# Kernel optimization log

Measured on AMD Instinct MI355X. Metric: run time of the kernel, lower is better.

The kernel has to match this reference:

```python
import jax, jax.numpy as jnp
import numpy as np

N, E, G = 50000, 800000, 512
F_IN, ED, NUM_CLASSES = 128, 3, 10
H1, C1, C2 = 4, 32, 64


def _add_self_loops(src, dst, eattr, n):
    # PyG add_self_loops with fill_value='mean': loop attr = mean of incoming edge attrs
    cnt = jax.ops.segment_sum(jnp.ones_like(dst, dtype=eattr.dtype), dst, num_segments=n)
    loop = jax.ops.segment_sum(eattr, dst, num_segments=n) / jnp.maximum(cnt, 1.0)[:, None]
    ar = jnp.arange(n)
    return (jnp.concatenate([src, ar]), jnp.concatenate([dst, ar]),
            jnp.concatenate([eattr, loop], axis=0))


def _gatv2(x, src, dst, eattr, Wl, bl, Wr, br, We, att, bias, heads, out_ch, concat, n):
    xl = (x @ Wl.T + bl).reshape(n, heads, out_ch)   # source transform (lin_l)
    xr = (x @ Wr.T + br).reshape(n, heads, out_ch)   # target transform (lin_r)
    ee = (eattr @ We.T).reshape(-1, heads, out_ch)   # edge transform (lin_edge, no bias)
    m = jax.nn.leaky_relu(xl[src] + xr[dst] + ee, 0.2)  # [E', H, C]
    score = jnp.einsum('ehc,hc->eh', m, att)
    # segment softmax over incoming edges of each target node
    smax = jax.ops.segment_max(score, dst, num_segments=n)
    ex = jnp.exp(score - smax[dst])
    denom = jax.ops.segment_sum(ex, dst, num_segments=n)
    alpha = ex / denom[dst]
    out = jax.ops.segment_sum(alpha[:, :, None] * xl[src], dst, num_segments=n)
    out = out.reshape(n, heads * out_ch) if concat else out.mean(axis=1)
    return out + bias


def setup_inputs() -> dict:
    key = jax.random.key(0)
    ks = jax.random.split(key, 24)
    s = 0.1
    return {
        'x': jax.random.normal(ks[0], (N, F_IN), jnp.float32),
        'edge_index': jax.random.randint(ks[1], (2, E), 0, N),
        'edge_attr': jax.random.normal(ks[2], (E, ED), jnp.float32),
        'batch': jnp.sort(jax.random.randint(ks[3], (N,), 0, G)),
        'u': jax.random.normal(ks[4], (G, 1), jnp.float32),
        'Wl1': jax.random.normal(ks[5], (H1 * C1, F_IN), jnp.float32) * s,
        'bl1': jnp.zeros((H1 * C1,), jnp.float32),
        'Wr1': jax.random.normal(ks[6], (H1 * C1, F_IN), jnp.float32) * s,
        'br1': jnp.zeros((H1 * C1,), jnp.float32),
        'We1': jax.random.normal(ks[7], (H1 * C1, ED), jnp.float32) * s,
        'att1': jax.random.normal(ks[8], (H1, C1), jnp.float32) * s,
        'b1': jnp.zeros((H1 * C1,), jnp.float32),
        'Wl2': jax.random.normal(ks[9], (C2, H1 * C1), jnp.float32) * s,
        'bl2': jnp.zeros((C2,), jnp.float32),
        'Wr2': jax.random.normal(ks[10], (C2, H1 * C1), jnp.float32) * s,
        'br2': jnp.zeros((C2,), jnp.float32),
        'We2': jax.random.normal(ks[11], (C2, ED), jnp.float32) * s,
        'att2': jax.random.normal(ks[12], (1, C2), jnp.float32) * s,
        'b2': jnp.zeros((C2,), jnp.float32),
        'W_lin1': jax.random.normal(ks[13], (32, 65), jnp.float32) * s,
        'b_lin1': jnp.zeros((32,), jnp.float32),
        'W_head': jax.random.normal(ks[14], (NUM_CLASSES, 32), jnp.float32) * s,
        'b_head': jnp.zeros((NUM_CLASSES,), jnp.float32),
    }


def reference(x, edge_index, edge_attr, batch, u,
              Wl1, bl1, Wr1, br1, We1, att1, b1,
              Wl2, bl2, Wr2, br2, We2, att2, b2,
              W_lin1, b_lin1, W_head, b_head):
    n = x.shape[0]
    src, dst, ea = _add_self_loops(edge_index[0], edge_index[1], edge_attr, n)
    h = jax.nn.elu(_gatv2(x, src, dst, ea, Wl1, bl1, Wr1, br1, We1, att1, b1, H1, C1, True, n))
    h = jax.nn.elu(_gatv2(h, src, dst, ea, Wl2, bl2, Wr2, br2, We2, att2, b2, 1, C2, False, n))
    cnt = jax.ops.segment_sum(jnp.ones((n,), h.dtype), batch, num_segments=G)
    pooled = jax.ops.segment_sum(h, batch, num_segments=G) / jnp.maximum(cnt, 1.0)[:, None]
    z = jax.nn.relu(jnp.concatenate([pooled, u], axis=1) @ W_lin1.T + b_lin1)
    return z @ W_head.T + b_head
```

## Files before the change

### kernel.cpp

```cpp
#include <hip/hip_runtime.h>
#include <hip/hip_fp16.h>
#include <math.h>


union H2U { __half2 h; unsigned u; };
typedef _Float16 hv2_t __attribute__((ext_vector_type(2)));
typedef unsigned uv4_t __attribute__((ext_vector_type(4)));

__device__ __forceinline__ __half2 hmax2(__half2 a, __half2 b) {
  union { __half2 h; hv2_t v; } x, y, r;
  x.h = a; y.h = b;
  r.v = __builtin_elementwise_max(x.v, y.v);
  return r.h;
}

#if __has_builtin(__builtin_amdgcn_fdot2)
__device__ __forceinline__ float dot2f(__half2 a, __half2 b, float c) {
  union { __half2 h; hv2_t v; } x, y;
  x.h = a; y.h = b;
  return __builtin_amdgcn_fdot2(x.v, y.v, c, false);
}
#else
__device__ __forceinline__ float dot2f(__half2 a, __half2 b, float c) {
  float2 af = __half22float2(a), bf = __half22float2(b);
  return fmaf(af.x, bf.x, fmaf(af.y, bf.y, c));
}
#endif

#if __has_builtin(__builtin_amdgcn_exp2f)
__device__ __forceinline__ float fexp2(float x) { return __builtin_amdgcn_exp2f(x); }
#else
__device__ __forceinline__ float fexp2(float x) { return exp2f(x); }
#endif

#if __has_builtin(__builtin_amdgcn_update_dpp)
template <int CTRL>
__device__ __forceinline__ float dpp_add(float v) {
  int r = __builtin_amdgcn_update_dpp(0, __builtin_bit_cast(int, v),
                                      CTRL, 0xf, 0xf, true);
  return v + __builtin_bit_cast(float, r);
}
__device__ __forceinline__ float row_sum16(float v) {
  v = dpp_add<0x121>(v);
  v = dpp_add<0x122>(v);
  v = dpp_add<0x124>(v);
  v = dpp_add<0x128>(v);
  return v;
}
#else
__device__ __forceinline__ float row_sum16(float v) {
  v += __shfl_xor(v, 1);
  v += __shfl_xor(v, 2);
  v += __shfl_xor(v, 4);
  v += __shfl_xor(v, 8);
  return v;
}
#endif

__device__ __forceinline__ float lowf(unsigned u) {
  H2U t; t.u = u;
  return __half2float(__low2half(t.h));
}

#define LOG2E 1.44269504088896f

__global__ void hist_k(const int* __restrict__ dst, int* __restrict__ deg,
                       int* __restrict__ rank, int E) {
  int e = blockIdx.x * 256 + threadIdx.x;
  if (e < E) rank[e] = atomicAdd(&deg[dst[e]], 1);
}

__global__ void blocksum_k(const int* __restrict__ deg, int* __restrict__ bsum, int N) {
  __shared__ int s[256];
  int i = blockIdx.x * 256 + threadIdx.x;
  s[threadIdx.x] = (i < N) ? deg[i] : 0;
  __syncthreads();
  for (int off = 128; off; off >>= 1) {
    if (threadIdx.x < off) s[threadIdx.x] += s[threadIdx.x + off];
    __syncthreads();
  }
  if (threadIdx.x == 0) bsum[blockIdx.x] = s[0];
}

__global__ void writeptr_k(const int* __restrict__ deg, const int* __restrict__ bsum,
                           int* __restrict__ rowptr, int N, int E) {
  __shared__ int s[256];
  __shared__ int bs[256];
  int t = threadIdx.x;
  int i = blockIdx.x * 256 + t;
  bs[t] = (t < (int)blockIdx.x) ? bsum[t] : 0;
  s[t] = (i < N) ? deg[i] : 0;
  __syncthreads();
  for (int off = 128; off; off >>= 1) {
    if (t < off) bs[t] += bs[t + off];
    __syncthreads();
  }
  int base = bs[0];
  __syncthreads();
  for (int off = 1; off < 256; off <<= 1) {
    int v = (t >= off) ? s[t - off] : 0;
    __syncthreads();
    if (t >= off) s[t] += v;
    __syncthreads();
  }
  int excl = base + ((t == 0) ? 0 : s[t - 1]) + i;
  if (i < N) rowptr[i] = excl;
  if (i == N - 1) rowptr[N] = E + N;
}

__global__ void fill_k(const int* __restrict__ src, const int* __restrict__ dst,
                       const float* __restrict__ eattr, const int* __restrict__ rowptr,
                       const int* __restrict__ rank, uint4* __restrict__ erec, int E) {
  int e = blockIdx.x * 256 + threadIdx.x;
  if (e >= E) return;
  int pos = rowptr[dst[e]] + rank[e];
  H2U a0, a1, a2;
  float e0 = eattr[e * 3 + 0], e1 = eattr[e * 3 + 1], e2 = eattr[e * 3 + 2];
  a0.h = __floats2half2_rn(e0, e0);
  a1.h = __floats2half2_rn(e1, e1);
  a2.h = __floats2half2_rn(e2, e2);
  uv4_t v = {(unsigned)src[e], a0.u, a1.u, a2.u};
  __builtin_nontemporal_store(v, (uv4_t*)&erec[pos]);
}

__global__ void loopattr_k(const int* __restrict__ rowptr, uint4* __restrict__ erec, int N) {
  int lane = threadIdx.x & 63;
  int n = (int)((blockIdx.x * 256 + threadIdx.x) >> 6);
  if (n >= N) return;
  int beg = rowptr[n], endr = rowptr[n + 1] - 1;
  float f0 = 0.f, f1 = 0.f, f2 = 0.f;
  for (int i = beg + lane; i < endr; i += 64) {
    uint4 r = erec[i];
    f0 += lowf(r.y);
    f1 += lowf(r.z);
    f2 += lowf(r.w);
  }
#pragma unroll
  for (int off = 1; off < 64; off <<= 1) {
    f0 += __shfl_xor(f0, off);
    f1 += __shfl_xor(f1, off);
    f2 += __shfl_xor(f2, off);
  }
  if (lane == 0) {
    float inv = 1.0f / fmaxf((float)(endr - beg), 1.0f);
    H2U a0, a1, a2;
    a0.h = __floats2half2_rn(f0 * inv, f0 * inv);
    a1.h = __floats2half2_rn(f1 * inv, f1 * inv);
    a2.h = __floats2half2_rn(f2 * inv, f2 * inv);
    erec[endr] = make_uint4((unsigned)n, a0.u, a1.u, a2.u);
  }
}

template <int J>
__global__ __launch_bounds__(256) void node_linear2t_k(
    const float* __restrict__ X,
    const float* __restrict__ W1, const float* __restrict__ b1v,
    const float* __restrict__ W2, const float* __restrict__ b2v,
    __half* __restrict__ out1, __half* __restrict__ out2, int nrows) {
  constexpr int K = 128, KB = 32;
  constexpr int JG = J / 4;
  constexpr int RG = 256 / JG;
  constexpr int RB = RG * 8;
  constexpr int XP2 = RB + 4;
  constexpr int WP2 = J + 4;
  __shared__ __align__(16) __half2 sXT2[K / 2][XP2];
  __shared__ __align__(16) __half2 sW1T2[KB / 2][WP2];
  __shared__ __align__(16) __half2 sW2T2[KB / 2][WP2];

  int tid = threadIdx.x;
  int n0 = blockIdx.x * RB;

  {
    int r = tid & (RB - 1);
    constexpr int KQSX = 256 / RB;
    int n = n0 + r;
    bool ok = n < nrows;
    for (int kq = tid / RB; kq < K / 4; kq += KQSX) {
      float4 v = ok ? *(const float4*)&X[(size_t)n * K + kq * 4]
                    : make_float4(0.f, 0.f, 0.f, 0.f);
      sXT2[kq * 2 + 0][r] = __floats2half2_rn(v.x, v.y);
      sXT2[kq * 2 + 1][r] = __floats2half2_rn(v.z, v.w);
    }
  }

  int jg = tid % JG;
  int rg = tid / JG;
  float acc1[8][4] = {}, acc2[8][4] = {};

  for (int kb = 0; kb < K / KB; ++kb) {
    __syncthreads();
    {
      int j = tid & (J - 1);
      constexpr int KQS = 256 / J;
      for (int kq = tid / J; kq < KB / 4; kq += KQS) {
        float4 v1 = *(const float4*)&W1[(size_t)j * K + kb * KB + kq * 4];
        float4 v2 = *(const float4*)&W2[(size_t)j * K + kb * KB + kq * 4];
        sW1T2[kq * 2 + 0][j] = __floats2half2_rn(v1.x, v1.y);
        sW1T2[kq * 2 + 1][j] = __floats2half2_rn(v1.z, v1.w);
        sW2T2[kq * 2 + 0][j] = __floats2half2_rn(v2.x, v2.y);
        sW2T2[kq * 2 + 1][j] = __floats2half2_rn(v2.z, v2.w);
      }
    }
    __syncthreads();
#pragma unroll
    for (int k2 = 0; k2 < KB / 2; ++k2) {
      __half2 xs2[8], w1s2[4], w2s2[4];
      *(float4*)&xs2[0] = *(const float4*)&sXT2[kb * (KB / 2) + k2][rg * 8];
      *(float4*)&xs2[4] = *(const float4*)&sXT2[kb * (KB / 2) + k2][rg * 8 + 4];
      *(float4*)w1s2 = *(const float4*)&sW1T2[k2][jg * 4];
      *(float4*)w2s2 = *(const float4*)&sW2T2[k2][jg * 4];
#pragma unroll
      for (int i = 0; i < 8; ++i)
#pragma unroll
        for (int q = 0; q < 4; ++q) {
          acc1[i][q] = dot2f(xs2[i], w1s2[q], acc1[i][q]);
          acc2[i][q] = dot2f(xs2[i], w2s2[q], acc2[i][q]);
        }
    }
  }

  float4 bv1 = *(const float4*)&b1v[jg * 4];
  float4 bv2 = *(const float4*)&b2v[jg * 4];
#pragma unroll
  for (int i = 0; i < 8; ++i) {
    int n = n0 + rg * 8 + i;
    if (n < nrows) {
      H2U a, b, c, d;
      a.h = __floats2half2_rn(acc1[i][0] + bv1.x, acc1[i][1] + bv1.y);
      b.h = __floats2half2_rn(acc1[i][2] + bv1.z, acc1[i][3] + bv1.w);
      *(uint2*)&out1[(size_t)n * J + jg * 4] = make_uint2(a.u, b.u);
      c.h = __floats2half2_rn(acc2[i][0] + bv2.x, acc2[i][1] + bv2.y);
      d.h = __floats2half2_rn(acc2[i][2] + bv2.z, acc2[i][3] + bv2.w);
      *(uint2*)&out2[(size_t)n * J + jg * 4] = make_uint2(c.u, d.u);
    }
  }
}

__global__ __launch_bounds__(128) void gat1_fused_k(
    const int* __restrict__ rowptr, const uint4* __restrict__ erec,
    const __half* __restrict__ xlh, const __half* __restrict__ xrh,
    const float* __restrict__ We, const float* __restrict__ att,
    const float* __restrict__ bias, float* __restrict__ out, int N) {
  constexpr int CH = 8;
  int lane = threadIdx.x & 63;
  int wave0 = __builtin_amdgcn_readfirstlane(
      (int)((blockIdx.x * blockDim.x + threadIdx.x) >> 6));
  int nwaves = (gridDim.x * blockDim.x) >> 6;
  const __half2* xl2p = (const __half2*)xlh;
  const __half2* xr2p = (const __half2*)xrh;
  int c0 = 2 * lane;
  __half2 w0p = __floats2half2_rn(We[c0 * 3 + 0], We[c0 * 3 + 3]);
  __half2 w1p = __floats2half2_rn(We[c0 * 3 + 1], We[c0 * 3 + 4]);
  __half2 w2p = __floats2half2_rn(We[c0 * 3 + 2], We[c0 * 3 + 5]);
  __half2 attp = __floats2half2_rn(att[c0] * LOG2E, att[c0 + 1] * LOG2E);
  __half2 k02 = __floats2half2_rn(0.2f, 0.2f);
  float2 bv = make_float2(bias[c0], bias[c0 + 1]);

  for (int n = wave0; n < N; n += nwaves) {
    __half2 xrp = xr2p[(size_t)n * 64 + lane];
    int beg = rowptr[n], end = rowptr[n + 1];
    int cnt = end - beg;

    float acc0 = 0.f, acc1 = 0.f, den = 0.f;

    int nfull = cnt / CH;
    for (int ch = 0; ch < nfull; ++ch) {
      int b = beg + ch * CH;
      uint4 recs[CH];
#pragma unroll
      for (int j = 0; j < CH; ++j) recs[j] = erec[b + j];
      __half2 r_[CH];
#pragma unroll
      for (int j = 0; j < CH; ++j) {
        int s = __builtin_amdgcn_readfirstlane((int)recs[j].x);
        r_[j] = xl2p[(size_t)s * 64 + lane];
      }
#pragma unroll
      for (int j = 0; j < CH; ++j) {
        H2U e0, e1, e2;
        e0.u = recs[j].y; e1.u = recs[j].z; e2.u = recs[j].w;
        __half2 m = __hadd2(r_[j], xrp);
        m = __hfma2(e0.h, w0p, m);
        m = __hfma2(e1.h, w1p, m);
        m = __hfma2(e2.h, w2p, m);
        m = hmax2(m, __hmul2(m, k02));
        float v = row_sum16(dot2f(m, attp, 0.f));
        float ex = fexp2(v);
        float2 rfF = __half22float2(r_[j]);
        den += ex;
        acc0 = fmaf(ex, rfF.x, acc0);
        acc1 = fmaf(ex, rfF.y, acc1);
      }
    }
    int gi = beg + nfull * CH;
    for (; gi + 2 <= end; gi += 2) {
      uint4 recA = erec[gi];
      uint4 recB = erec[gi + 1];
      int sA = __builtin_amdgcn_readfirstlane((int)recA.x);
      int sB = __builtin_amdgcn_readfirstlane((int)recB.x);
      __half2 rfA = xl2p[(size_t)sA * 64 + lane];
      __half2 rfB = xl2p[(size_t)sB * 64 + lane];
      {
        H2U e0, e1, e2;
        e0.u = recA.y; e1.u = recA.z; e2.u = recA.w;
        __half2 m = __hadd2(rfA, xrp);
        m = __hfma2(e0.h, w0p, m);
        m = __hfma2(e1.h, w1p, m);
        m = __hfma2(e2.h, w2p, m);
        m = hmax2(m, __hmul2(m, k02));
        float v = row_sum16(dot2f(m, attp, 0.f));
        float ex = fexp2(v);
        float2 rfF = __half22float2(rfA);
        den += ex;
        acc0 = fmaf(ex, rfF.x, acc0);
        acc1 = fmaf(ex, rfF.y, acc1);
      }
      {
        H2U e0, e1, e2;
        e0.u = recB.y; e1.u = recB.z; e2.u = recB.w;
        __half2 m = __hadd2(rfB, xrp);
        m = __hfma2(e0.h, w0p, m);
        m = __hfma2(e1.h, w1p, m);
        m = __hfma2(e2.h, w2p, m);
        m = hmax2(m, __hmul2(m, k02));
        float v = row_sum16(dot2f(m, attp, 0.f));
        float ex = fexp2(v);
        float2 rfF = __half22float2(rfB);
        den += ex;
        acc0 = fmaf(ex, rfF.x, acc0);
        acc1 = fmaf(ex, rfF.y, acc1);
      }
    }
    if (gi < end) {
      uint4 rec = erec[gi];
      int s = __builtin_amdgcn_readfirstlane((int)rec.x);
      __half2 rf = xl2p[(size_t)s * 64 + lane];
      H2U e0, e1, e2;
      e0.u = rec.y; e1.u = rec.z; e2.u = rec.w;
      __half2 m = __hadd2(rf, xrp);
      m = __hfma2(e0.h, w0p, m);
      m = __hfma2(e1.h, w1p, m);
      m = __hfma2(e2.h, w2p, m);
      m = hmax2(m, __hmul2(m, k02));
      float v = row_sum16(dot2f(m, attp, 0.f));
      float ex = fexp2(v);
      float2 rfF = __half22float2(rf);
      den += ex;
      acc0 = fmaf(ex, rfF.x, acc0);
      acc1 = fmaf(ex, rfF.y, acc1);
    }

    float o0 = acc0 / den + bv.x;
    float o1 = acc1 / den + bv.y;
    o0 = o0 > 0.f ? o0 : __expf(o0) - 1.0f;
    o1 = o1 > 0.f ? o1 : __expf(o1) - 1.0f;
    *(float2*)&out[(size_t)n * 128 + c0] = make_float2(o0, o1);
  }
}

__global__ __launch_bounds__(128) void gat2_fused_k(
    const int* __restrict__ rowptr, const uint4* __restrict__ erec,
    const __half* __restrict__ xlh, const __half* __restrict__ xrh,
    const float* __restrict__ We, const float* __restrict__ att,
    const float* __restrict__ bias, float* __restrict__ out, int N) {
  constexpr int CP = 4;
  int lane = threadIdx.x & 63;
  int wave0 = __builtin_amdgcn_readfirstlane(
      (int)((blockIdx.x * blockDim.x + threadIdx.x) >> 6));
  int nwaves = (gridDim.x * blockDim.x) >> 6;
  int sub = lane & 31, grp = lane >> 5;
  int c0 = 2 * sub;
  const __half2* xl2p = (const __half2*)xlh;
  const __half2* xr2p = (const __half2*)xrh;
  __half2 w0p = __floats2half2_rn(We[c0 * 3 + 0], We[c0 * 3 + 3]);
  __half2 w1p = __floats2half2_rn(We[c0 * 3 + 1], We[c0 * 3 + 4]);
  __half2 w2p = __floats2half2_rn(We[c0 * 3 + 2], We[c0 * 3 + 5]);
  __half2 attp = __floats2half2_rn(att[c0] * LOG2E, att[c0 + 1] * LOG2E);
  __half2 k02 = __floats2half2_rn(0.2f, 0.2f);
  float2 bv = make_float2(bias[c0], bias[c0 + 1]);

  for (int n = wave0; n < N; n += nwaves) {
    __half2 xrp = xr2p[(size_t)n * 32 + sub];
    int beg = rowptr[n], end = rowptr[n + 1];
    int cnt = end - beg;

    float acc0 = 0.f, acc1 = 0.f, den = 0.f;

    int nfull = cnt / (2 * CP);
    int b = beg + grp;
    for (int ch = 0; ch < nfull; ++ch) {
      uint4 recs[CP];
      __half2 r_[CP];
#pragma unroll
      for (int j = 0; j < CP; ++j) recs[j] = erec[b + 2 * j];
#pragma unroll
      for (int j = 0; j < CP; ++j) r_[j] = xl2p[(size_t)recs[j].x * 32 + sub];
#pragma unroll
      for (int j = 0; j < CP; ++j) {
        H2U e0, e1, e2;
        e0.u = recs[j].y; e1.u = recs[j].z; e2.u = recs[j].w;
        __half2 m = __hadd2(r_[j], xrp);
        m = __hfma2(e0.h, w0p, m);
        m = __hfma2(e1.h, w1p, m);
        m = __hfma2(e2.h, w2p, m);
        m = hmax2(m, __hmul2(m, k02));
        float v = row_sum16(dot2f(m, attp, 0.f));
        v += __shfl_xor(v, 16);
        float ex = fexp2(v);
        float2 rfF = __half22float2(r_[j]);
        den += ex;
        acc0 = fmaf(ex, rfF.x, acc0);
        acc1 = fmaf(ex, rfF.y, acc1);
      }
      b += 2 * CP;
    }
    for (int gi = beg + nfull * 2 * CP + grp; gi < end; gi += 2) {
      uint4 rec = erec[gi];
      __half2 rf = xl2p[(size_t)rec.x * 32 + sub];
      H2U e0, e1, e2;
      e0.u = rec.y; e1.u = rec.z; e2.u = rec.w;
      __half2 m = __hadd2(rf, xrp);
      m = __hfma2(e0.h, w0p, m);
      m = __hfma2(e1.h, w1p, m);
      m = __hfma2(e2.h, w2p, m);
      m = hmax2(m, __hmul2(m, k02));
      float v = row_sum16(dot2f(m, attp, 0.f));
      v += __shfl_xor(v, 16);
      float ex = fexp2(v);
      float2 rfF = __half22float2(rf);
      den += ex;
      acc0 = fmaf(ex, rfF.x, acc0);
      acc1 = fmaf(ex, rfF.y, acc1);
    }

    acc0 += __shfl_xor(acc0, 32);
    acc1 += __shfl_xor(acc1, 32);
    den += __shfl_xor(den, 32);

    if (grp == 0) {
      float o0 = acc0 / den + bv.x;
      float o1 = acc1 / den + bv.y;
      o0 = o0 > 0.f ? o0 : __expf(o0) - 1.0f;
      o1 = o1 > 0.f ? o1 : __expf(o1) - 1.0f;
      *(float2*)&out[(size_t)n * 64 + c0] = make_float2(o0, o1);
    }
  }
}

__global__ void final_mlp_k(const float* __restrict__ h2, const int* __restrict__ batch,
                            int N, const float* __restrict__ u,
                            const float* __restrict__ W1, const float* __restrict__ b1,
                            const float* __restrict__ Wh, const float* __restrict__ bh,
                            float* __restrict__ out) {
  __shared__ float comb[4][64];
  __shared__ float feat[65];
  __shared__ float z[32];
  int g = blockIdx.x;
  int t = threadIdx.x;
  int c = t & 63, q = t >> 6;
  int lo, hi;
  {
    int l = 0, h = N;
    while (l < h) { int m = (l + h) >> 1; if (batch[m] < g) l = m + 1; else h = m; }
    lo = l;
    h = N;
    while (l < h) { int m = (l + h) >> 1; if (batch[m] < g + 1) l = m + 1; else h = m; }
    hi = l;
  }
  float a = 0.f;
  for (int nn = lo + q; nn < hi; nn += 4) a += h2[(size_t)nn * 64 + c];
  comb[q][c] = a;
  __syncthreads();
  if (t < 64) {
    float s = comb[0][t] + comb[1][t] + comb[2][t] + comb[3][t];
    float inv = 1.0f / fmaxf((float)(hi - lo), 1.0f);
    feat[t] = s * inv;
    if (t == 0) feat[64] = u[g];
  }
  __syncthreads();
  if (t < 32) {
    float s = b1[t];
    for (int k = 0; k < 65; ++k) s += feat[k] * W1[t * 65 + k];
    z[t] = fmaxf(s, 0.0f);
  }
  __syncthreads();
  if (t < 10) {
    float s = bh[t];
    for (int k = 0; k < 32; ++k) s += z[k] * Wh[t * 32 + k];
    out[g * 10 + t] = s;
  }
}

extern "C" void kernel_launch(void* const* d_in, const int* in_sizes, int n_in,
                              void* d_out, int out_size, void* d_ws, size_t ws_size,
                              hipStream_t stream) {
  const float* x      = (const float*)d_in[0];
  const int*   eidx   = (const int*)d_in[1];
  const float* eattr  = (const float*)d_in[2];
  const int*   batch  = (const int*)d_in[3];
  const float* u      = (const float*)d_in[4];
  const float* Wl1    = (const float*)d_in[5];
  const float* bl1    = (const float*)d_in[6];
  const float* Wr1    = (const float*)d_in[7];
  const float* br1    = (const float*)d_in[8];
  const float* We1    = (const float*)d_in[9];
  const float* att1   = (const float*)d_in[10];
  const float* b1     = (const float*)d_in[11];
  const float* Wl2    = (const float*)d_in[12];
  const float* bl2    = (const float*)d_in[13];
  const float* Wr2    = (const float*)d_in[14];
  const float* br2    = (const float*)d_in[15];
  const float* We2    = (const float*)d_in[16];
  const float* att2   = (const float*)d_in[17];
  const float* b2     = (const float*)d_in[18];
  const float* W_lin1 = (const float*)d_in[19];
  const float* b_lin1 = (const float*)d_in[20];
  const float* W_head = (const float*)d_in[21];
  const float* b_head = (const float*)d_in[22];

  const int N = in_sizes[0] / 128;
  const int E = in_sizes[1] / 2;
  const int G = in_sizes[4];
  const int* srcp = eidx;
  const int* dstp = eidx + E;

  __half* bufh = (__half*)d_ws;
  __half* bufr = bufh + (size_t)N * 128;
  float* buf3 = (float*)(bufr + (size_t)N * 128);
  uint4* erec = (uint4*)(buf3 + (size_t)N * 128);
  int* rank   = (int*)(erec + ((size_t)E + N));
  int* deg    = rank + E;
  int* rowptr = deg + N;
  int* bsum   = rowptr + N + 1;

  const int nb = (N + 255) / 256;
  const int gat_blocks = (N + 1) / 2;

  (void)hipMemsetAsync(deg, 0, sizeof(int) * (size_t)N, stream);
  hist_k<<<(E + 255) / 256, 256, 0, stream>>>(dstp, deg, rank, E);
  blocksum_k<<<nb, 256, 0, stream>>>(deg, bsum, N);
  writeptr_k<<<nb, 256, 0, stream>>>(deg, bsum, rowptr, N, E);
  fill_k<<<(E + 255) / 256, 256, 0, stream>>>(srcp, dstp, eattr, rowptr, rank, erec, E);
  loopattr_k<<<(N * 64 + 255) / 256, 256, 0, stream>>>(rowptr, erec, N);

  node_linear2t_k<128><<<(N + 63) / 64, 256, 0, stream>>>(x, Wl1, bl1, Wr1, br1,
                                                          bufh, bufr, N);
  gat1_fused_k<<<gat_blocks, 128, 0, stream>>>(rowptr, erec, bufh, bufr,
                                               We1, att1, b1, buf3, N);

  node_linear2t_k<64><<<(N + 127) / 128, 256, 0, stream>>>(buf3, Wl2, bl2, Wr2, br2,
                                                           bufh, bufr, N);
  gat2_fused_k<<<gat_blocks, 128, 0, stream>>>(rowptr, erec, bufh, bufr,
                                               We2, att2, b2, buf3, N);

  final_mlp_k<<<G, 256, 0, stream>>>(buf3, batch, N, u, W_lin1, b_lin1, W_head, b_head,
                                     (float*)d_out);
}
```

Before: 366.2 us.

## Replace dot2 node linear kernels with MFMA fp16 matmuls and half-precision intermediates

Replaces the shared-memory dot2-based dual linear kernel with an MFMA 16x16x32 fp16 kernel that reads fp16 inputs and fp16 pre-converted weights straight from global memory. Extra kernels convert x and the four weight matrices to fp16 beforehand. The first GAT layer now writes its output in fp16, which halves that buffer's traffic and removes a conversion for the second linear. The layer-1 linear moves before the CSR build. The cost is extra launches, scattered 2-byte output stores, and more fp16 rounding of the intermediate activations.

```diff
diff --git a/kernel.cpp b/kernel.cpp
--- a/kernel.cpp
+++ b/kernel.cpp
@@ -6,6 +6,8 @@
 union H2U { __half2 h; unsigned u; };
 typedef _Float16 hv2_t __attribute__((ext_vector_type(2)));
 typedef unsigned uv4_t __attribute__((ext_vector_type(4)));
+typedef _Float16 f16x8 __attribute__((ext_vector_type(8)));
+typedef float f32x4 __attribute__((ext_vector_type(4)));
 
 __device__ __forceinline__ __half2 hmax2(__half2 a, __half2 b) {
   union { __half2 h; hv2_t v; } x, y, r;
@@ -151,87 +153,106 @@
   }
 }
 
+__global__ void cvt_f32_f16_k(const float* __restrict__ src, __half* __restrict__ dst,
+                              int n8) {
+  int i = blockIdx.x * 256 + threadIdx.x;
+  if (i >= n8) return;
+  const float4* s = (const float4*)(src + (size_t)i * 8);
+  float4 v0 = s[0], v1 = s[1];
+  H2U h0, h1, h2, h3;
+  h0.h = __floats2half2_rn(v0.x, v0.y);
+  h1.h = __floats2half2_rn(v0.z, v0.w);
+  h2.h = __floats2half2_rn(v1.x, v1.y);
+  h3.h = __floats2half2_rn(v1.z, v1.w);
+  uv4_t o = {h0.u, h1.u, h2.u, h3.u};
+  *(uv4_t*)(dst + (size_t)i * 8) = o;
+}
+
+__global__ void cvt_w_all_k(const float* __restrict__ Wl1, const float* __restrict__ Wr1,
+                            const float* __restrict__ Wl2, const float* __restrict__ Wr2,
+                            __half* __restrict__ wh1, __half* __restrict__ wh2) {
+  int i = blockIdx.x * 256 + threadIdx.x;
+  if (i >= 6144) return;
+  const float* s;
+  __half* d;
+  int off;
+  if (i < 2048)      { s = Wl1; d = wh1;         off = i; }
+  else if (i < 4096) { s = Wr1; d = wh1 + 16384; off = i - 2048; }
+  else if (i < 5120) { s = Wl2; d = wh2;         off = i - 4096; }
+  else               { s = Wr2; d = wh2 + 8192;  off = i - 5120; }
+  const float4* sp = (const float4*)(s + (size_t)off * 8);
+  float4 v0 = sp[0], v1 = sp[1];
+  H2U h0, h1, h2, h3;
+  h0.h = __floats2half2_rn(v0.x, v0.y);
+  h1.h = __floats2half2_rn(v0.z, v0.w);
+  h2.h = __floats2half2_rn(v1.x, v1.y);
+  h3.h = __floats2half2_rn(v1.z, v1.w);
+  uv4_t o = {h0.u, h1.u, h2.u, h3.u};
+  *(uv4_t*)(d + (size_t)off * 8) = o;
+}
+
 template <int J>
-__global__ __launch_bounds__(256) void node_linear2t_k(
-    const float* __restrict__ X,
-    const float* __restrict__ W1, const float* __restrict__ b1v,
-    const float* __restrict__ W2, const float* __restrict__ b2v,
-    __half* __restrict__ out1, __half* __restrict__ out2, int nrows) {
-  constexpr int K = 128, KB = 32;
-  constexpr int JG = J / 4;
-  constexpr int RG = 256 / JG;
-  constexpr int RB = RG * 8;
-  constexpr int XP2 = RB + 4;
-  constexpr int WP2 = J + 4;
-  __shared__ __align__(16) __half2 sXT2[K / 2][XP2];
-  __shared__ __align__(16) __half2 sW1T2[KB / 2][WP2];
-  __shared__ __align__(16) __half2 sW2T2[KB / 2][WP2];
-
-  int tid = threadIdx.x;
-  int n0 = blockIdx.x * RB;
-
-  {
-    int r = tid & (RB - 1);
-    constexpr int KQSX = 256 / RB;
-    int n = n0 + r;
-    bool ok = n < nrows;
-    for (int kq = tid / RB; kq < K / 4; kq += KQSX) {
-      float4 v = ok ? *(const float4*)&X[(size_t)n * K + kq * 4]
-                    : make_float4(0.f, 0.f, 0.f, 0.f);
-      sXT2[kq * 2 + 0][r] = __floats2half2_rn(v.x, v.y);
-      sXT2[kq * 2 + 1][r] = __floats2half2_rn(v.z, v.w);
-    }
-  }
-
-  int jg = tid % JG;
-  int rg = tid / JG;
-  float acc1[8][4] = {}, acc2[8][4] = {};
-
-  for (int kb = 0; kb < K / KB; ++kb) {
-    __syncthreads();
-    {
-      int j = tid & (J - 1);
-      constexpr int KQS = 256 / J;
-      for (int kq = tid / J; kq < KB / 4; kq += KQS) {
-        float4 v1 = *(const float4*)&W1[(size_t)j * K + kb * KB + kq * 4];
-        float4 v2 = *(const float4*)&W2[(size_t)j * K + kb * KB + kq * 4];
-        sW1T2[kq * 2 + 0][j] = __floats2half2_rn(v1.x, v1.y);
-        sW1T2[kq * 2 + 1][j] = __floats2half2_rn(v1.z, v1.w);
-        sW2T2[kq * 2 + 0][j] = __floats2half2_rn(v2.x, v2.y);
-        sW2T2[kq * 2 + 1][j] = __floats2half2_rn(v2.z, v2.w);
-      }
-    }
-    __syncthreads();
-#pragma unroll
-    for (int k2 = 0; k2 < KB / 2; ++k2) {
-      __half2 xs2[8], w1s2[4], w2s2[4];
-      *(float4*)&xs2[0] = *(const float4*)&sXT2[kb * (KB / 2) + k2][rg * 8];
-      *(float4*)&xs2[4] = *(const float4*)&sXT2[kb * (KB / 2) + k2][rg * 8 + 4];
-      *(float4*)w1s2 = *(const float4*)&sW1T2[k2][jg * 4];
-      *(float4*)w2s2 = *(const float4*)&sW2T2[k2][jg * 4];
-#pragma unroll
-      for (int i = 0; i < 8; ++i)
-#pragma unroll
-        for (int q = 0; q < 4; ++q) {
-          acc1[i][q] = dot2f(xs2[i], w1s2[q], acc1[i][q]);
-          acc2[i][q] = dot2f(xs2[i], w2s2[q], acc2[i][q]);
-        }
-    }
-  }
-
-  float4 bv1 = *(const float4*)&b1v[jg * 4];
-  float4 bv2 = *(const float4*)&b2v[jg * 4];
-#pragma unroll
-  for (int i = 0; i < 8; ++i) {
-    int n = n0 + rg * 8 + i;
-    if (n < nrows) {
-      H2U a, b, c, d;
-      a.h = __floats2half2_rn(acc1[i][0] + bv1.x, acc1[i][1] + bv1.y);
-      b.h = __floats2half2_rn(acc1[i][2] + bv1.z, acc1[i][3] + bv1.w);
-      *(uint2*)&out1[(size_t)n * J + jg * 4] = make_uint2(a.u, b.u);
-      c.h = __floats2half2_rn(acc2[i][0] + bv2.x, acc2[i][1] + bv2.y);
-      d.h = __floats2half2_rn(acc2[i][2] + bv2.z, acc2[i][3] + bv2.w);
-      *(uint2*)&out2[(size_t)n * J + jg * 4] = make_uint2(c.u, d.u);
+__global__ __launch_bounds__(256) void mfma_linear2_k(
+    const __half* __restrict__ Xh, const __half* __restrict__ Wh,
+    const float* __restrict__ b1v, const float* __restrict__ b2v,
+    __half* __restrict__ out1, __half* __restrict__ out2, int N) {
+  constexpr int CG = (2 * J) / 64;
+  int lane = threadIdx.x & 63;
+  int wid = __builtin_amdgcn_readfirstlane(
+      (int)((blockIdx.x * 256 + threadIdx.x) >> 6));
+  int rt = wid / CG;
+  int cg = wid - rt * CG;
+  int r0 = rt * 32;
+  if (r0 >= N) return;
+
+  int koff = (lane >> 4) * 8;
+  int row0 = r0 + (lane & 15);
+  int row1 = row0 + 16;
+  int cr0 = min(row0, N - 1), cr1 = min(row1, N - 1);
+
+  const __half* xp0 = Xh + (size_t)cr0 * 128 + koff;
+  const __half* xp1 = Xh + (size_t)cr1 * 128 + koff;
+  f16x8 a0[4], a1[4];
+#pragma unroll
+  for (int ks = 0; ks < 4; ++ks) {
+    a0[ks] = *(const f16x8*)(xp0 + ks * 32);
+    a1[ks] = *(const f16x8*)(xp1 + ks * 32);
+  }
+
+  bool isT1 = (cg * 64) < J;
+  const float* bt = isT1 ? b1v : b2v;
+  __half* op = isT1 ? out1 : out2;
+  int cbase = cg * 64 - (isT1 ? 0 : J);
+  int cl = cbase + (lane & 15);
+  int rA = r0 + ((lane >> 4) << 2);
+
+#pragma unroll
+  for (int ct = 0; ct < 4; ++ct) {
+    int col = cg * 64 + ct * 16 + (lane & 15);
+    const __half* wp = Wh + (size_t)col * 128 + koff;
+    f16x8 b0 = *(const f16x8*)(wp);
+    f16x8 b1_ = *(const f16x8*)(wp + 32);
+    f16x8 b2_ = *(const f16x8*)(wp + 64);
+    f16x8 b3_ = *(const f16x8*)(wp + 96);
+    f32x4 acc0 = {0.f, 0.f, 0.f, 0.f};
+    f32x4 acc1 = {0.f, 0.f, 0.f, 0.f};
+    acc0 = __builtin_amdgcn_mfma_f32_16x16x32_f16(a0[0], b0, acc0, 0, 0, 0);
+    acc1 = __builtin_amdgcn_mfma_f32_16x16x32_f16(a1[0], b0, acc1, 0, 0, 0);
+    acc0 = __builtin_amdgcn_mfma_f32_16x16x32_f16(a0[1], b1_, acc0, 0, 0, 0);
+    acc1 = __builtin_amdgcn_mfma_f32_16x16x32_f16(a1[1], b1_, acc1, 0, 0, 0);
+    acc0 = __builtin_amdgcn_mfma_f32_16x16x32_f16(a0[2], b2_, acc0, 0, 0, 0);
+    acc1 = __builtin_amdgcn_mfma_f32_16x16x32_f16(a1[2], b2_, acc1, 0, 0, 0);
+    acc0 = __builtin_amdgcn_mfma_f32_16x16x32_f16(a0[3], b3_, acc0, 0, 0, 0);
+    acc1 = __builtin_amdgcn_mfma_f32_16x16x32_f16(a1[3], b3_, acc1, 0, 0, 0);
+
+    int cc = cl + ct * 16;
+    float bb = bt[cc];
+#pragma unroll
+    for (int q = 0; q < 4; ++q) {
+      int r = rA + q;
+      if (r < N) op[(size_t)r * J + cc] = __float2half(acc0[q] + bb);
+      int r2 = r + 16;
+      if (r2 < N) op[(size_t)r2 * J + cc] = __float2half(acc1[q] + bb);
     }
   }
 }
@@ -240,7 +261,7 @@
     const int* __restrict__ rowptr, const uint4* __restrict__ erec,
     const __half* __restrict__ xlh, const __half* __restrict__ xrh,
     const float* __restrict__ We, const float* __restrict__ att,
-    const float* __restrict__ bias, float* __restrict__ out, int N) {
+    const float* __restrict__ bias, __half* __restrict__ out, int N) {
   constexpr int CH = 8;
   int lane = threadIdx.x & 63;
   int wave0 = __builtin_amdgcn_readfirstlane(
@@ -248,6 +269,7 @@
   int nwaves = (gridDim.x * blockDim.x) >> 6;
   const __half2* xl2p = (const __half2*)xlh;
   const __half2* xr2p = (const __half2*)xrh;
+  __half2* outp = (__half2*)out;
   int c0 = 2 * lane;
   __half2 w0p = __floats2half2_rn(We[c0 * 3 + 0], We[c0 * 3 + 3]);
   __half2 w1p = __floats2half2_rn(We[c0 * 3 + 1], We[c0 * 3 + 4]);
@@ -354,7 +376,9 @@
     float o1 = acc1 / den + bv.y;
     o0 = o0 > 0.f ? o0 : __expf(o0) - 1.0f;
     o1 = o1 > 0.f ? o1 : __expf(o1) - 1.0f;
-    *(float2*)&out[(size_t)n * 128 + c0] = make_float2(o0, o1);
+    H2U o;
+    o.h = __floats2half2_rn(o0, o1);
+    outp[(size_t)n * 64 + lane] = o.h;
   }
 }
 
@@ -527,14 +551,25 @@
   __half* bufh = (__half*)d_ws;
   __half* bufr = bufh + (size_t)N * 128;
   float* buf3 = (float*)(bufr + (size_t)N * 128);
+  __half* g1h = (__half*)buf3;
+  float* h2f = (float*)(g1h + (size_t)N * 128);
   uint4* erec = (uint4*)(buf3 + (size_t)N * 128);
+  __half* xh  = (__half*)erec;
   int* rank   = (int*)(erec + ((size_t)E + N));
   int* deg    = rank + E;
   int* rowptr = deg + N;
   int* bsum   = rowptr + N + 1;
+  uintptr_t wtop = ((uintptr_t)(bsum + 256) + 15) & ~(uintptr_t)15;
+  __half* wh1 = (__half*)wtop;
+  __half* wh2 = wh1 + 32768;
 
   const int nb = (N + 255) / 256;
   const int gat_blocks = (N + 1) / 2;
+  const int rt = (N + 31) / 32;
+
+  cvt_w_all_k<<<24, 256, 0, stream>>>(Wl1, Wr1, Wl2, Wr2, wh1, wh2);
+  cvt_f32_f16_k<<<(N * 16 + 255) / 256, 256, 0, stream>>>(x, xh, N * 16);
+  mfma_linear2_k<128><<<rt, 256, 0, stream>>>(xh, wh1, bl1, br1, bufh, bufr, N);
 
   (void)hipMemsetAsync(deg, 0, sizeof(int) * (size_t)N, stream);
   hist_k<<<(E + 255) / 256, 256, 0, stream>>>(dstp, deg, rank, E);
@@ -543,16 +578,14 @@
   fill_k<<<(E + 255) / 256, 256, 0, stream>>>(srcp, dstp, eattr, rowptr, rank, erec, E);
   loopattr_k<<<(N * 64 + 255) / 256, 256, 0, stream>>>(rowptr, erec, N);
 
-  node_linear2t_k<128><<<(N + 63) / 64, 256, 0, stream>>>(x, Wl1, bl1, Wr1, br1,
-                                                          bufh, bufr, N);
   gat1_fused_k<<<gat_blocks, 128, 0, stream>>>(rowptr, erec, bufh, bufr,
-                                               We1, att1, b1, buf3, N);
-
-  node_linear2t_k<64><<<(N + 127) / 128, 256, 0, stream>>>(buf3, Wl2, bl2, Wr2, br2,
+                                               We1, att1, b1, g1h, N);
+
+  mfma_linear2_k<64><<<(rt * 2 + 3) / 4, 256, 0, stream>>>(g1h, wh2, bl2, br2,
                                                            bufh, bufr, N);
   gat2_fused_k<<<gat_blocks, 128, 0, stream>>>(rowptr, erec, bufh, bufr,
-                                               We2, att2, b2, buf3, N);
-
-  final_mlp_k<<<G, 256, 0, stream>>>(buf3, batch, N, u, W_lin1, b_lin1, W_head, b_head,
+                                               We2, att2, b2, h2f, N);
+
+  final_mlp_k<<<G, 256, 0, stream>>>(h2f, batch, N, u, W_lin1, b_lin1, W_head, b_head,
                                      (float*)d_out);
 }
```

New measurement: 338.2 us. 1.08x faster.
